# Performance work log

Measured on AMD Instinct MI355X. Metric: run time of the kernel, lower is better.

Reference implementation:

```python
import jax, jax.numpy as jnp
import numpy as np

NUM_HEADS = 16


def setup_inputs() -> dict:
    key = jax.random.key(0)
    k1, k2, k3 = jax.random.split(key, 3)
    B, N, C = 2, 2048, 1024
    x = jax.random.normal(k1, (B, N, C), dtype=jnp.float32)
    w_qkv = jax.random.normal(k2, (3 * C, C), dtype=jnp.float32) * (C ** -0.5)
    w_proj = jax.random.normal(k3, (C, C), dtype=jnp.float32) * (C ** -0.5)
    b_proj = jnp.zeros((C,), dtype=jnp.float32)
    return {"x": x, "w_qkv": w_qkv, "w_proj": w_proj, "b_proj": b_proj}


def reference(x, w_qkv, w_proj, b_proj):
    B, N, C = x.shape
    H = NUM_HEADS
    D = C // H
    scale = 1.0 / jnp.sqrt(jnp.asarray(D, x.dtype))
    qkv = (x @ w_qkv.T).reshape(B, N, 3, H, D)
    qkv = jnp.transpose(qkv, (2, 0, 3, 1, 4))  # [3,B,H,N,D]
    q, k, v = qkv[0], qkv[1], qkv[2]
    # scaled dot-product attention with explicit score matrix [B,H,N,N]
    attn = jnp.einsum('bhnd,bhmd->bhnm', q, k) * scale
    attn = jax.nn.softmax(attn, axis=-1)
    out = jnp.einsum('bhnm,bhmd->bhnd', attn, v)
    out = jnp.transpose(out, (0, 2, 1, 3)).reshape(B, N, C)
    # output projection
    return out @ w_proj.T + b_proj
```

## Files before the change

### kernel.cpp

```cpp
#include <hip/hip_runtime.h>

typedef unsigned short u16;
typedef __attribute__((ext_vector_type(8))) short bf16x8;
typedef __attribute__((ext_vector_type(4))) float f32x4;

#define B_ 2
#define N_ 2048
#define C_ 1024
#define H_ 16
#define D_ 64
#define M_ (B_ * N_)

#define QSCALE 0.18033688011114336f

__device__ __forceinline__ u16 f2bf(float f) {
    union { float f; unsigned u; } x; x.f = f;
    return (u16)((x.u + 0x8000u) >> 16);
}
__device__ __forceinline__ unsigned pack2bf(float a, float b) {
    union { float f; unsigned u; } x, y; x.f = a; y.f = b;
    return __builtin_amdgcn_perm(y.u + 0x8000u, x.u + 0x8000u, 0x07060302);
}

__device__ __forceinline__ void async_copy16(const void* gsrc, void* ldst) {
    __builtin_amdgcn_global_load_lds(
        (__attribute__((address_space(1))) void*)gsrc,
        (__attribute__((address_space(3))) void*)ldst,
        16, 0, 0);
}

__global__ void cast3_kernel(const float* __restrict__ x, const float* __restrict__ wq,
                             const float* __restrict__ wp, u16* __restrict__ xo,
                             u16* __restrict__ wqo, u16* __restrict__ wpo) {
    int b = blockIdx.x;
    const float* s; u16* d;
    if (b < 4096)      { s = x;  d = xo;  }
    else if (b < 7168) { s = wq; d = wqo; b -= 4096; }
    else               { s = wp; d = wpo; b -= 7168; }
    int i = (b * 256 + threadIdx.x) * 4;
    const float4 v = *(const float4*)(s + i);
    uint2 o;
    o.x = pack2bf(v.x, v.y);
    o.y = pack2bf(v.z, v.w);
    *(uint2*)(d + i) = o;
}

template <int EPI>
__global__ __launch_bounds__(256, 2) void gemm_bt(
    const u16* __restrict__ A, const u16* __restrict__ Bm,
    int M, int Ncols, int K, int ntiles_n,
    u16* __restrict__ qo, u16* __restrict__ ko, u16* __restrict__ vo,
    const float* __restrict__ bias, float* __restrict__ out) {
    __shared__ u16 As[128 * 64];
    __shared__ u16 Bs[128 * 64];
    const int tid = threadIdx.x, lane = tid & 63, w = tid >> 6;
    const int bx = blockIdx.x % ntiles_n, by = blockIdx.x / ntiles_n;
    const int m0 = by * 128, n0 = bx * 128;
    const int wm = w >> 1, wn = w & 1;
    const int q16 = lane >> 4, l15 = lane & 15;
    const int r0 = lane >> 3, c0 = (lane & 7) * 8;
    f32x4 acc[4][4] = {};

    for (int k0 = 0; k0 < K; k0 += 64) {
#pragma unroll
        for (int i = 0; i < 4; ++i) {
            int blk = w * 4 + i;
            int r = blk * 8 + r0;
            async_copy16(A + (size_t)(m0 + r) * K + k0 + c0, (char*)As + blk * 1024);
            async_copy16(Bm + (size_t)(n0 + r) * K + k0 + c0, (char*)Bs + blk * 1024);
        }
        __builtin_amdgcn_s_waitcnt(0);
        __syncthreads();
#pragma unroll
        for (int ks = 0; ks < 2; ++ks) {
            bf16x8 af[4], bf[4];
#pragma unroll
            for (int i = 0; i < 4; ++i) {
                af[i] = *(const bf16x8*)&As[(wm * 64 + i * 16 + l15) * 64 + ks * 32 + q16 * 8];
                bf[i] = *(const bf16x8*)&Bs[(wn * 64 + i * 16 + l15) * 64 + ks * 32 + q16 * 8];
            }
#pragma unroll
            for (int mi = 0; mi < 4; ++mi)
#pragma unroll
                for (int ni = 0; ni < 4; ++ni)
                    acc[mi][ni] = __builtin_amdgcn_mfma_f32_16x16x32_bf16(af[mi], bf[ni], acc[mi][ni], 0, 0, 0);
        }
        __syncthreads();
    }

#pragma unroll
    for (int mi = 0; mi < 4; ++mi) {
#pragma unroll
        for (int ni = 0; ni < 4; ++ni) {
            int n_g = n0 + wn * 64 + ni * 16 + l15;
#pragma unroll
            for (int r = 0; r < 4; ++r) {
                int m_g = m0 + wm * 64 + mi * 16 + q16 * 4 + r;
                float v = acc[mi][ni][r];
                if (EPI == 0) {
                    int which = n_g >> 10;
                    int h = (n_g >> 6) & 15;
                    int d = n_g & 63;
                    int b = m_g >> 11;
                    int nn = m_g & 2047;
                    size_t idx = ((size_t)((b * H_ + h) * N_ + nn) << 6) + d;
                    if (which == 0)      qo[idx] = f2bf(v * QSCALE);
                    else if (which == 1) ko[idx] = f2bf(v);
                    else                 vo[idx] = f2bf(v);
                } else {
                    out[(size_t)m_g * Ncols + n_g] = v + bias[n_g];
                }
            }
        }
    }
}

__global__ __launch_bounds__(256) void transpose_v(const u16* __restrict__ V, u16* __restrict__ VT) {
    __shared__ u16 tile[64][72];
    const int t = threadIdx.x;
    const int bh = blockIdx.x >> 5;
    const int key0 = (blockIdx.x & 31) * 64;
    const size_t base = (size_t)bh * N_ * D_;
    const int r0 = t >> 3, c8 = (t & 7) * 8;
#pragma unroll
    for (int it = 0; it < 2; ++it) {
        int r = it * 32 + r0;
        uint4 d4 = *(const uint4*)(V + base + (size_t)(key0 + r) * D_ + c8);
        *(uint4*)&tile[r][c8] = d4;
    }
    __syncthreads();
#pragma unroll
    for (int it = 0; it < 2; ++it) {
        int d = it * 32 + r0;
        unsigned t0 = tile[c8 + 0][d], t1 = tile[c8 + 1][d], t2 = tile[c8 + 2][d], t3 = tile[c8 + 3][d];
        unsigned t4 = tile[c8 + 4][d], t5 = tile[c8 + 5][d], t6 = tile[c8 + 6][d], t7 = tile[c8 + 7][d];
        uint4 o;
        o.x = t0 | (t1 << 16); o.y = t2 | (t3 << 16);
        o.z = t4 | (t5 << 16); o.w = t6 | (t7 << 16);
        *(uint4*)(VT + base + (size_t)d * N_ + key0 + c8) = o;
    }
}

__global__ __launch_bounds__(256, 3) void attn_kernel(
    const u16* __restrict__ Q, const u16* __restrict__ K,
    const u16* __restrict__ VT, u16* __restrict__ O) {
    __shared__ u16 Qs[64 * 64];
    __shared__ u16 Ks[128 * 64];
    __shared__ u16 Vs[64 * 128];
    __shared__ u16 Ps[4][16 * 68];
    const int tid = threadIdx.x, lane = tid & 63, w = tid >> 6;
    const int q16 = lane >> 4, l15 = lane & 15;
    const int l7 = l15 & 7;
    const int bh = blockIdx.x >> 5;
    const int q0 = (blockIdx.x & 31) * 64;
    const size_t head = (size_t)bh * N_ * D_;
    const int lr3 = lane >> 3, lc7 = lane & 7;
    const int lr4 = lane >> 4, lc15 = lane & 15;

#pragma unroll
    for (int i = 0; i < 2; ++i) {
        int blk = w * 2 + i;
        int row = blk * 8 + lr3;
        async_copy16(Q + head + (size_t)(q0 + row) * D_ + (lc7 ^ lr3) * 8, (char*)Qs + blk * 1024);
    }
    __builtin_amdgcn_s_waitcnt(0);
    __syncthreads();
    bf16x8 qf[2];
#pragma unroll
    for (int ks = 0; ks < 2; ++ks)
        qf[ks] = *(const bf16x8*)&Qs[(w * 16 + l15) * 64 + ((ks * 4 + q16) ^ l7) * 8];

    f32x4 o_acc[4] = {};
    float rs = 0.f;

    for (int kt = 0; kt < 16; ++kt) {
        int key0 = kt * 128;
#pragma unroll
        for (int i = 0; i < 4; ++i) {
            int c = w * 4 + i;
            int krow = c * 8 + lr3;
            async_copy16(K + head + (size_t)(key0 + krow) * D_ + (lc7 ^ lr3) * 8,
                         (char*)Ks + c * 1024);
            int vrow = c * 4 + lr4;
            async_copy16(VT + head + (size_t)vrow * N_ + key0 + (lc15 ^ (vrow & 15)) * 8,
                         (char*)Vs + c * 1024);
        }
        __builtin_amdgcn_s_waitcnt(0);
        __syncthreads();

#pragma unroll
        for (int half = 0; half < 2; ++half) {
#pragma unroll
            for (int kb = 0; kb < 4; ++kb) {
                f32x4 st = {};
#pragma unroll
                for (int ks = 0; ks < 2; ++ks) {
                    bf16x8 kf = *(const bf16x8*)&Ks[((half * 4 + kb) * 16 + l15) * 64 + ((ks * 4 + q16) ^ l7) * 8];
                    st = __builtin_amdgcn_mfma_f32_16x16x32_bf16(kf, qf[ks], st, 0, 0, 0);
                }
                float p0 = exp2f(st[0]), p1 = exp2f(st[1]), p2 = exp2f(st[2]), p3 = exp2f(st[3]);
                rs += (p0 + p1) + (p2 + p3);
                uint2 pk;
                pk.x = pack2bf(p0, p1);
                pk.y = pack2bf(p2, p3);
                *(uint2*)&Ps[w][l15 * 68 + kb * 16 + q16 * 4] = pk;
            }
#pragma unroll
            for (int ks2 = 0; ks2 < 2; ++ks2) {
                bf16x8 pf = *(const bf16x8*)&Ps[w][l15 * 68 + ks2 * 32 + q16 * 8];
#pragma unroll
                for (int di = 0; di < 4; ++di) {
                    bf16x8 vf = *(const bf16x8*)&Vs[(di * 16 + l15) * 128 + (((half * 2 + ks2) * 4 + q16) ^ l15) * 8];
                    o_acc[di] = __builtin_amdgcn_mfma_f32_16x16x32_bf16(pf, vf, o_acc[di], 0, 0, 0);
                }
            }
        }
        __syncthreads();
    }

    rs += __shfl_xor(rs, 16);
    rs += __shfl_xor(rs, 32);
    float inv[4];
#pragma unroll
    for (int r = 0; r < 4; ++r) inv[r] = 1.0f / __shfl(rs, q16 * 4 + r);

    const int b = bh >> 4, h = bh & 15;
#pragma unroll
    for (int di = 0; di < 4; ++di) {
        int d = di * 16 + l15;
#pragma unroll
        for (int r = 0; r < 4; ++r) {
            int qg = q0 + w * 16 + q16 * 4 + r;
            O[((size_t)(b * N_ + qg) << 10) + h * 64 + d] = f2bf(o_acc[di][r] * inv[r]);
        }
    }
}

extern "C" void kernel_launch(void* const* d_in, const int* in_sizes, int n_in,
                              void* d_out, int out_size, void* d_ws, size_t ws_size,
                              hipStream_t stream) {
    const float* x      = (const float*)d_in[0];
    const float* w_qkv  = (const float*)d_in[1];
    const float* w_proj = (const float*)d_in[2];
    const float* b_proj = (const float*)d_in[3];
    float* out = (float*)d_out;

    char* ws = (char*)d_ws;
    const size_t MB = 1024 * 1024;
    u16* x_bf     = (u16*)(ws + 0 * MB);
    u16* wqkv_bf  = (u16*)(ws + 8 * MB);
    u16* wproj_bf = (u16*)(ws + 14 * MB);
    u16* q_bf     = (u16*)(ws + 16 * MB);
    u16* k_bf     = (u16*)(ws + 24 * MB);
    u16* v_bf     = (u16*)(ws + 32 * MB);
    u16* vt_bf    = (u16*)(ws + 40 * MB);
    u16* ao_bf    = (u16*)(ws + 48 * MB);

    cast3_kernel<<<8192, 256, 0, stream>>>(x, w_qkv, w_proj, x_bf, wqkv_bf, wproj_bf);

    gemm_bt<0><<<32 * 24, 256, 0, stream>>>(x_bf, wqkv_bf, M_, 3 * C_, C_, 24,
                                            q_bf, k_bf, v_bf, nullptr, nullptr);

    transpose_v<<<1024, 256, 0, stream>>>(v_bf, vt_bf);

    attn_kernel<<<1024, 256, 0, stream>>>(q_bf, k_bf, vt_bf, ao_bf);

    gemm_bt<1><<<32 * 8, 256, 0, stream>>>(ao_bf, wproj_bf, M_, C_, C_, 8,
                                           nullptr, nullptr, nullptr, b_proj, out);
}
```

Measured before the change: 211.6 us.

## Double query rows per attention block to reuse K/V tiles across two fragments

Each attention block now handles 128 query rows instead of 64, with each wave computing two 16-row fragments that share every K and V fragment read from LDS. This halves the grid and the global K/V traffic per query, and amortizes LDS reads across more MFMAs. In exchange it raises register and LDS use, lowers the occupancy hint from 3 to 2 blocks per CU, and leaves only 512 blocks, which may leave the 256 CUs less evenly loaded.

Result: no change. 210.3 us (-0.6%).

```diff
diff --git a/kernel.cpp b/kernel.cpp
--- a/kernel.cpp
+++ b/kernel.cpp
@@ -141,37 +141,39 @@
     }
 }
 
-__global__ __launch_bounds__(256, 3) void attn_kernel(
+__global__ __launch_bounds__(256, 2) void attn_kernel(
     const u16* __restrict__ Q, const u16* __restrict__ K,
     const u16* __restrict__ VT, u16* __restrict__ O) {
-    __shared__ u16 Qs[64 * 64];
+    __shared__ u16 Qs[128 * 64];
     __shared__ u16 Ks[128 * 64];
     __shared__ u16 Vs[64 * 128];
-    __shared__ u16 Ps[4][16 * 68];
+    __shared__ u16 Ps[4][32 * 68];
     const int tid = threadIdx.x, lane = tid & 63, w = tid >> 6;
     const int q16 = lane >> 4, l15 = lane & 15;
     const int l7 = l15 & 7;
-    const int bh = blockIdx.x >> 5;
-    const int q0 = (blockIdx.x & 31) * 64;
+    const int bh = blockIdx.x >> 4;
+    const int q0 = (blockIdx.x & 15) * 128;
     const size_t head = (size_t)bh * N_ * D_;
     const int lr3 = lane >> 3, lc7 = lane & 7;
     const int lr4 = lane >> 4, lc15 = lane & 15;
 
 #pragma unroll
-    for (int i = 0; i < 2; ++i) {
-        int blk = w * 2 + i;
-        int row = blk * 8 + lr3;
-        async_copy16(Q + head + (size_t)(q0 + row) * D_ + (lc7 ^ lr3) * 8, (char*)Qs + blk * 1024);
+    for (int i = 0; i < 4; ++i) {
+        int c = w * 4 + i;
+        int row = c * 8 + lr3;
+        async_copy16(Q + head + (size_t)(q0 + row) * D_ + (lc7 ^ lr3) * 8, (char*)Qs + c * 1024);
     }
     __builtin_amdgcn_s_waitcnt(0);
     __syncthreads();
-    bf16x8 qf[2];
-#pragma unroll
-    for (int ks = 0; ks < 2; ++ks)
-        qf[ks] = *(const bf16x8*)&Qs[(w * 16 + l15) * 64 + ((ks * 4 + q16) ^ l7) * 8];
-
-    f32x4 o_acc[4] = {};
-    float rs = 0.f;
+    bf16x8 qf[2][2];
+#pragma unroll
+    for (int f = 0; f < 2; ++f)
+#pragma unroll
+        for (int ks = 0; ks < 2; ++ks)
+            qf[f][ks] = *(const bf16x8*)&Qs[(w * 32 + f * 16 + l15) * 64 + ((ks * 4 + q16) ^ l7) * 8];
+
+    f32x4 o_acc[2][4] = {};
+    float rs[2] = {0.f, 0.f};
 
     for (int kt = 0; kt < 16; ++kt) {
         int key0 = kt * 128;
@@ -192,46 +194,63 @@
         for (int half = 0; half < 2; ++half) {
 #pragma unroll
             for (int kb = 0; kb < 4; ++kb) {
-                f32x4 st = {};
+                f32x4 st[2] = {};
 #pragma unroll
                 for (int ks = 0; ks < 2; ++ks) {
                     bf16x8 kf = *(const bf16x8*)&Ks[((half * 4 + kb) * 16 + l15) * 64 + ((ks * 4 + q16) ^ l7) * 8];
-                    st = __builtin_amdgcn_mfma_f32_16x16x32_bf16(kf, qf[ks], st, 0, 0, 0);
-                }
-                float p0 = exp2f(st[0]), p1 = exp2f(st[1]), p2 = exp2f(st[2]), p3 = exp2f(st[3]);
-                rs += (p0 + p1) + (p2 + p3);
-                uint2 pk;
-                pk.x = pack2bf(p0, p1);
-                pk.y = pack2bf(p2, p3);
-                *(uint2*)&Ps[w][l15 * 68 + kb * 16 + q16 * 4] = pk;
+#pragma unroll
+                    for (int f = 0; f < 2; ++f)
+                        st[f] = __builtin_amdgcn_mfma_f32_16x16x32_bf16(kf, qf[f][ks], st[f], 0, 0, 0);
+                }
+#pragma unroll
+                for (int f = 0; f < 2; ++f) {
+                    float p0 = exp2f(st[f][0]), p1 = exp2f(st[f][1]);
+                    float p2 = exp2f(st[f][2]), p3 = exp2f(st[f][3]);
+                    rs[f] += (p0 + p1) + (p2 + p3);
+                    uint2 pk;
+                    pk.x = pack2bf(p0, p1);
+                    pk.y = pack2bf(p2, p3);
+                    *(uint2*)&Ps[w][(f * 16 + l15) * 68 + kb * 16 + q16 * 4] = pk;
+                }
             }
 #pragma unroll
             for (int ks2 = 0; ks2 < 2; ++ks2) {
-                bf16x8 pf = *(const bf16x8*)&Ps[w][l15 * 68 + ks2 * 32 + q16 * 8];
+                bf16x8 pf[2];
+#pragma unroll
+                for (int f = 0; f < 2; ++f)
+                    pf[f] = *(const bf16x8*)&Ps[w][(f * 16 + l15) * 68 + ks2 * 32 + q16 * 8];
 #pragma unroll
                 for (int di = 0; di < 4; ++di) {
                     bf16x8 vf = *(const bf16x8*)&Vs[(di * 16 + l15) * 128 + (((half * 2 + ks2) * 4 + q16) ^ l15) * 8];
-                    o_acc[di] = __builtin_amdgcn_mfma_f32_16x16x32_bf16(pf, vf, o_acc[di], 0, 0, 0);
-                }
-            }
-        }
-        __syncthreads();
-    }
-
-    rs += __shfl_xor(rs, 16);
-    rs += __shfl_xor(rs, 32);
-    float inv[4];
-#pragma unroll
-    for (int r = 0; r < 4; ++r) inv[r] = 1.0f / __shfl(rs, q16 * 4 + r);
+#pragma unroll
+                    for (int f = 0; f < 2; ++f)
+                        o_acc[f][di] = __builtin_amdgcn_mfma_f32_16x16x32_bf16(pf[f], vf, o_acc[f][di], 0, 0, 0);
+                }
+            }
+        }
+        __syncthreads();
+    }
+
+#pragma unroll
+    for (int f = 0; f < 2; ++f) {
+        rs[f] += __shfl_xor(rs[f], 16);
+        rs[f] += __shfl_xor(rs[f], 32);
+    }
 
     const int b = bh >> 4, h = bh & 15;
 #pragma unroll
-    for (int di = 0; di < 4; ++di) {
-        int d = di * 16 + l15;
-#pragma unroll
-        for (int r = 0; r < 4; ++r) {
-            int qg = q0 + w * 16 + q16 * 4 + r;
-            O[((size_t)(b * N_ + qg) << 10) + h * 64 + d] = f2bf(o_acc[di][r] * inv[r]);
+    for (int f = 0; f < 2; ++f) {
+        float inv[4];
+#pragma unroll
+        for (int r = 0; r < 4; ++r) inv[r] = 1.0f / __shfl(rs[f], q16 * 4 + r);
+#pragma unroll
+        for (int di = 0; di < 4; ++di) {
+            int d = di * 16 + l15;
+#pragma unroll
+            for (int r = 0; r < 4; ++r) {
+                int qg = q0 + w * 32 + f * 16 + q16 * 4 + r;
+                O[((size_t)(b * N_ + qg) << 10) + h * 64 + d] = f2bf(o_acc[f][di][r] * inv[r]);
+            }
         }
     }
 }
@@ -263,7 +282,7 @@
 
     transpose_v<<<1024, 256, 0, stream>>>(v_bf, vt_bf);
 
-    attn_kernel<<<1024, 256, 0, stream>>>(q_bf, k_bf, vt_bf, ao_bf);
+    attn_kernel<<<512, 256, 0, stream>>>(q_bf, k_bf, vt_bf, ao_bf);
 
     gemm_bt<1><<<32 * 8, 256, 0, stream>>>(ao_bf, wproj_bf, M_, C_, C_, 8,
                                            nullptr, nullptr, nullptr, b_proj, out);
```
